# Optimization experiments

Measured on AMD Instinct MI355X. Metric: run time of the kernel, lower is better.

The kernel has to match this reference:

```python
import jax, jax.numpy as jnp
import numpy as np

N_HEADS = 16
ROPE_BASE = 10000.0


def _rope_tables(T, head_dim, dtype):
    inv_freq = 1.0 / (ROPE_BASE ** (jnp.arange(0, head_dim, 2, dtype=jnp.float32) / head_dim))
    t = jnp.arange(T, dtype=jnp.float32)
    freqs = jnp.outer(t, inv_freq)              # (T, head_dim/2)
    emb = jnp.concatenate([freqs, freqs], -1)   # (T, head_dim)
    return jnp.cos(emb).astype(dtype), jnp.sin(emb).astype(dtype)


def _rotate_half(x):
    x1, x2 = jnp.split(x, 2, axis=-1)
    return jnp.concatenate([-x2, x1], axis=-1)


def setup_inputs() -> dict:
    key = jax.random.key(0)
    k1, k2, k3 = jax.random.split(key, 3)
    B, T, C = 2, 2048, 2048
    x = jax.random.normal(k1, (B, T, C), dtype=jnp.float32)
    Wqkv = jax.random.normal(k2, (C, 3 * C), dtype=jnp.float32) * (1.0 / np.sqrt(C))
    Wproj = jax.random.normal(k3, (C, C), dtype=jnp.float32) * (1.0 / np.sqrt(C))
    return {"x": x, "Wqkv": Wqkv, "Wproj": Wproj}


def reference(x, Wqkv, Wproj):
    B, T, C = x.shape
    H = N_HEADS
    D = C // H
    qkv = jnp.einsum('btc,cd->btd', x, Wqkv)            # (B,T,3C)
    q, k, v = jnp.split(qkv, 3, axis=-1)
    # (B,T,C) -> (B,H,T,D)
    q = q.reshape(B, T, H, D).transpose(0, 2, 1, 3)
    k = k.reshape(B, T, H, D).transpose(0, 2, 1, 3)
    v = v.reshape(B, T, H, D).transpose(0, 2, 1, 3)
    cos, sin = _rope_tables(T, D, x.dtype)              # (T,D) each
    q = q * cos + _rotate_half(q) * sin
    k = k * cos + _rotate_half(k) * sin
    scale = 1.0 / jnp.sqrt(jnp.asarray(D, x.dtype))
    att = jnp.einsum('bhqd,bhkd->bhqk', q, k) * scale   # (B,H,T,T)
    causal = jnp.tril(jnp.ones((T, T), dtype=bool))
    att = jnp.where(causal, att, jnp.asarray(-jnp.inf, att.dtype))
    att = jax.nn.softmax(att, axis=-1)
    y = jnp.einsum('bhqk,bhkd->bhqd', att, v)           # (B,H,T,D)
    y = y.transpose(0, 2, 1, 3).reshape(B, T, C)
    return jnp.einsum('btc,cd->btd', y, Wproj)
```

## Files before the change

kernel.cpp:

```cpp
#include <hip/hip_runtime.h>
#include <stdint.h>

#define T_SEQ 2048
#define NH 16
#define HD 128
#define CC 2048
#define N3 6144
#define MM 4096

typedef short bf16x8 __attribute__((ext_vector_type(8)));
typedef float f32x4 __attribute__((ext_vector_type(4)));
typedef float f32x16 __attribute__((ext_vector_type(16)));
typedef unsigned int u32x4 __attribute__((ext_vector_type(4)));

__device__ __forceinline__ unsigned short f2bf(float f) {
  unsigned int u = __float_as_uint(f);
  u += 0x7FFF + ((u >> 16) & 1);
  return (unsigned short)(u >> 16);
}
__device__ __forceinline__ float bf2f(unsigned short h) {
  return __uint_as_float(((unsigned int)h) << 16);
}
__device__ __forceinline__ unsigned int cvt_pk_bf16(float lo, float hi) {
  unsigned int r;
  asm("v_cvt_pk_bf16_f32 %0, %1, %2" : "=v"(r) : "v"(lo), "v"(hi));
  return r;
}

__global__ __launch_bounds__(256) void k_transpose_cvt(const float* __restrict__ in,
                                                       unsigned short* __restrict__ out,
                                                       int K, int N) {
  __shared__ float tile[32][33];
  int k0 = blockIdx.x * 32;
  int n0 = blockIdx.y * 32;
  int tx = threadIdx.x & 31, ty = threadIdx.x >> 5;
  #pragma unroll
  for (int r = ty; r < 32; r += 8)
    tile[r][tx] = in[(size_t)(k0 + r) * N + n0 + tx];
  __syncthreads();
  #pragma unroll
  for (int r = ty; r < 32; r += 8)
    out[(size_t)(n0 + r) * K + k0 + tx] = f2bf(tile[tx][r]);
}

__global__ __launch_bounds__(256) void k_cvt(const float* __restrict__ in,
                                             unsigned short* __restrict__ out, int n4) {
  int i = blockIdx.x * 256 + threadIdx.x;
  if (i >= n4) return;
  float4 v = ((const float4*)in)[i];
  ushort4 o;
  o.x = f2bf(v.x); o.y = f2bf(v.y); o.z = f2bf(v.z); o.w = f2bf(v.w);
  ((ushort4*)out)[i] = o;
}

template<int NJ, int EPI, int MMAJ>
__global__ __launch_bounds__(512, 1) void k_gemm8(const unsigned short* __restrict__ A,
                                                  const unsigned short* __restrict__ Bt,
                                                  float* __restrict__ C,
                                                  unsigned short* __restrict__ qo,
                                                  unsigned short* __restrict__ ko,
                                                  unsigned short* __restrict__ vo,
                                                  int M, int N, int K) {
  constexpr int BU = NJ / 2;
  constexpr int DSTRIDE = (1 + BU) * 16384;
  extern __shared__ __align__(16) char lds[];
  const int tid = threadIdx.x;
  const int lane = tid & 63;
  const int lr = lane & 15, lg = lane >> 4;
  const int wave = tid >> 6;
  const int wm = wave >> 2, wn = wave & 3;
  const int nwg = gridDim.x;
  const int bid = blockIdx.x;
  const int wg = (bid & 7) * (nwg >> 3) + (bid >> 3);
  const int GX = M >> 7;
  const int GN = N / (NJ * 64);
  const int mt = MMAJ ? (wg % GX) : (wg / GN);
  const int nt = MMAJ ? (wg / GX) : (wg % GN);
  const int m0 = mt * 128, n0 = nt * NJ * 64;
  const int NT = K >> 6;

  auto STAGE = [&](int d, int op, int h, int t) {
    const unsigned short* src = op ? Bt : A;
    const int r0 = (op ? n0 + h * 128 : m0);
    const int kc = t * 64;
    char* base = lds + d * DSTRIDE + op * 16384 + h * 16384;
    #pragma unroll
    for (int l = 0; l < 2; ++l) {
      int p = (l * 512 + tid) * 16;
      int qq = p ^ (((p >> 7) & 7) << 4);
      const unsigned short* g = src + (size_t)(r0 + (qq >> 7)) * K + kc + ((qq & 127) >> 1);
      __builtin_amdgcn_global_load_lds(
          (const __attribute__((address_space(1))) void*)g,
          (__attribute__((address_space(3))) void*)(base + (l * 512 + (tid & 448)) * 16),
          16, 0, 0);
    }
  };
  auto RD = [&](int d, int op, int row, int kb) -> bf16x8 {
    const char* base = lds + d * DSTRIDE + op * 16384;
    int p = row * 128 + kb;
    p ^= ((p >> 7) & 7) << 4;
    return *(const bf16x8*)(base + p);
  };

  f32x4 acc[4][NJ];
  #pragma unroll
  for (int i = 0; i < 4; ++i)
    #pragma unroll
    for (int j = 0; j < NJ; ++j) acc[i][j] = (f32x4){0.f, 0.f, 0.f, 0.f};

  bf16x8 bfrg[NJ][2];

#define PHASE(D, MIB, READB, VM, ...)                                                    \
  {                                                                                      \
    if (READB) {                                                                         \
      _Pragma("unroll")                                                                  \
      for (int nj = 0; nj < NJ; ++nj)                                                    \
        _Pragma("unroll")                                                                \
        for (int ks = 0; ks < 2; ++ks)                                                   \
          bfrg[nj][ks] = RD(D, 1, wn * NJ * 16 + nj * 16 + lr, ks * 64 + lg * 16);       \
    }                                                                                    \
    bf16x8 af2[2][2];                                                                    \
    _Pragma("unroll")                                                                    \
    for (int mm = 0; mm < 2; ++mm)                                                       \
      _Pragma("unroll")                                                                  \
      for (int ks = 0; ks < 2; ++ks)                                                     \
        af2[mm][ks] = RD(D, 0, wm * 64 + (MIB + mm) * 16 + lr, ks * 64 + lg * 16);       \
    __VA_ARGS__                                                                          \
    __builtin_amdgcn_s_barrier();                                                        \
    asm volatile("s_waitcnt lgkmcnt(0)" ::: "memory");                                   \
    __builtin_amdgcn_s_setprio(1);                                                       \
    _Pragma("unroll")                                                                    \
    for (int mm = 0; mm < 2; ++mm)                                                       \
      _Pragma("unroll")                                                                  \
      for (int nj = 0; nj < NJ; ++nj)                                                    \
        _Pragma("unroll")                                                                \
        for (int ks = 0; ks < 2; ++ks)                                                   \
          acc[MIB + mm][nj] = __builtin_amdgcn_mfma_f32_16x16x32_bf16(af2[mm][ks], bfrg[nj][ks], acc[MIB + mm][nj], 0, 0, 0); \
    __builtin_amdgcn_s_setprio(0);                                                       \
    if ((VM) == 6) asm volatile("s_waitcnt vmcnt(6)" ::: "memory");                      \
    if ((VM) == 4) asm volatile("s_waitcnt vmcnt(4)" ::: "memory");                      \
    if ((VM) == 2) asm volatile("s_waitcnt vmcnt(2)" ::: "memory");                      \
    __builtin_amdgcn_s_barrier();                                                        \
  }

  const int t1 = NT > 1 ? 1 : 0;
  #pragma unroll
  for (int h = 0; h < BU; ++h) STAGE(0, 1, h, 0);
  STAGE(0, 0, 0, 0);
  #pragma unroll
  for (int h = 0; h < BU; ++h) STAGE(1, 1, h, t1);
  if (NJ == 6) asm volatile("s_waitcnt vmcnt(6)" ::: "memory");
  else         asm volatile("s_waitcnt vmcnt(4)" ::: "memory");
  __builtin_amdgcn_s_barrier();

  for (int it = 0; it < (NT >> 1); ++it) {
    const int tb  = 2 * it + 1;
    const int ta1 = min(2 * it + 2, NT - 1);
    const int tb1 = min(2 * it + 3, NT - 1);
    if (NJ == 6) {
      PHASE(0, 0, true,  -1, STAGE(1, 0, 0, tb);)
      PHASE(0, 2, false,  4, STAGE(0, 1, 0, ta1); STAGE(0, 1, 1, ta1);)
      PHASE(1, 0, true,  -1, STAGE(0, 1, 2, ta1); STAGE(0, 0, 0, ta1);)
      PHASE(1, 2, false,  6, STAGE(1, 1, 0, tb1); STAGE(1, 1, 1, tb1); STAGE(1, 1, 2, tb1);)
    } else {
      PHASE(0, 0, true,  -1, STAGE(1, 0, 0, tb);)
      PHASE(0, 2, false,  2, STAGE(0, 1, 0, ta1);)
      PHASE(1, 0, true,  -1, STAGE(0, 1, 1, ta1); STAGE(0, 0, 0, ta1);)
      PHASE(1, 2, false,  4, STAGE(1, 1, 0, tb1); STAGE(1, 1, 1, tb1);)
    }
  }
#undef PHASE

  #pragma unroll
  for (int mi = 0; mi < 4; ++mi) {
    #pragma unroll
    for (int nj = 0; nj < NJ; ++nj) {
      #pragma unroll
      for (int j = 0; j < 4; ++j) {
        int m = m0 + wm * 64 + mi * 16 + lg * 4 + j;
        int n = n0 + wn * NJ * 16 + nj * 16 + lr;
        float val = acc[mi][nj][j];
        if (EPI == 0) {
          C[(size_t)m * N + n] = val;
        } else {
          int which = n >> 11, cc = n & 2047;
          int h = cc >> 7, d = cc & 127;
          int b = m >> 11, t = m & 2047;
          unsigned short* dst = which == 0 ? qo : (which == 1 ? ko : vo);
          dst[(((size_t)(b * NH + h)) * T_SEQ + t) * HD + d] = f2bf(val);
        }
      }
    }
  }
}

__global__ __launch_bounds__(256) void k_rope(unsigned short* __restrict__ q,
                                              unsigned short* __restrict__ k) {
  int i = blockIdx.x * 256 + threadIdx.x;
  int d = i & 63;
  int t = (i >> 6) & (T_SEQ - 1);
  int bh = i >> 17;
  float invf = exp2f((float)(-2 * d) * (13.287712379549449f / 128.f));
  float ang = (float)t * invf;
  float c = cosf(ang), s = sinf(ang);
  size_t base = ((size_t)bh * T_SEQ + t) * HD + d;
  const float scale = 0.12751741562076117f;
  float q1 = bf2f(q[base]), q2 = bf2f(q[base + 64]);
  q[base]      = f2bf((q1 * c - q2 * s) * scale);
  q[base + 64] = f2bf((q2 * c + q1 * s) * scale);
  float k1 = bf2f(k[base]), k2 = bf2f(k[base + 64]);
  k[base]      = f2bf(k1 * c - k2 * s);
  k[base + 64] = f2bf(k2 * c + k1 * s);
}

__global__ __launch_bounds__(256) void k_transpose_v(const unsigned short* __restrict__ in,
                                                     unsigned short* __restrict__ out) {
  __shared__ unsigned short tile[32][33];
  int bh = blockIdx.z;
  int t0 = blockIdx.x * 32, d0 = blockIdx.y * 32;
  int tx = threadIdx.x & 31, ty = threadIdx.x >> 5;
  const unsigned short* src = in + (size_t)bh * T_SEQ * HD;
  unsigned short* dst = out + (size_t)bh * HD * T_SEQ;
  #pragma unroll
  for (int r = ty; r < 32; r += 8)
    tile[r][tx] = src[(size_t)(t0 + r) * HD + d0 + tx];
  __syncthreads();
  #pragma unroll
  for (int r = ty; r < 32; r += 8)
    dst[(size_t)(d0 + r) * T_SEQ + t0 + tx] = tile[tx][r];
}

__global__ __launch_bounds__(256, 2) void k_attn(const unsigned short* __restrict__ Q,
                                                 const unsigned short* __restrict__ K,
                                                 const unsigned short* __restrict__ Vt,
                                                 unsigned short* __restrict__ Y) {
  __shared__ __align__(16) unsigned short Kls[2][64 * 128];
  __shared__ __align__(16) unsigned short Vls[2][128 * 64];
  const int id = blockIdx.x;
  const int sub = id & 255;
  const int bh = sub & 31;
  const int qtl = (id < 256) ? (15 - (sub >> 5)) : (sub >> 5);
  const int b = bh >> 4, h = bh & 15;
  const int tid = threadIdx.x, wv = tid >> 6, lane = tid & 63;
  const int l31 = lane & 31, hh = lane >> 5;
  const int q0 = qtl * 128;
  const int jtmax = 2 * qtl + 1;
  const int qglob = q0 + wv * 32 + l31;
  const unsigned short* Qb = Q + (size_t)bh * T_SEQ * HD;
  const unsigned short* Kb = K + (size_t)bh * T_SEQ * HD;
  const unsigned short* Vb = Vt + (size_t)bh * HD * T_SEQ;

  auto STAGEKV = [&](int tk, int bb) {
    #pragma unroll
    for (int ch = 0; ch < 4; ++ch) {
      int p = (ch * 256 + tid) * 16;
      int q = p ^ (((p >> 8) & 7) << 4);
      const unsigned short* g = Kb + (size_t)(tk + (q >> 8)) * HD + ((q & 255) >> 1);
      __builtin_amdgcn_global_load_lds(
          (const __attribute__((address_space(1))) void*)g,
          (__attribute__((address_space(3))) void*)((char*)Kls[bb] + (ch * 256 + (tid & 192)) * 16),
          16, 0, 0);
    }
    #pragma unroll
    for (int ch = 0; ch < 4; ++ch) {
      int p = (ch * 256 + tid) * 16;
      int q = p ^ (((p >> 7) & 7) << 4);
      const unsigned short* g = Vb + (size_t)(q >> 7) * T_SEQ + tk + ((q & 127) >> 1);
      __builtin_amdgcn_global_load_lds(
          (const __attribute__((address_space(1))) void*)g,
          (__attribute__((address_space(3))) void*)((char*)Vls[bb] + (ch * 256 + (tid & 192)) * 16),
          16, 0, 0);
    }
  };

  bf16x8 qfr[8];
  #pragma unroll
  for (int c = 0; c < 8; ++c)
    qfr[c] = *(const bf16x8*)(Qb + (size_t)qglob * HD + c * 16 + hh * 8);

  f32x16 oacc[4];
  #pragma unroll
  for (int dt = 0; dt < 4; ++dt)
    #pragma unroll
    for (int r = 0; r < 16; ++r) oacc[dt][r] = 0.f;
  float mrun = -1e30f, lrun = 0.f;

  STAGEKV(0, 0);
  asm volatile("s_waitcnt vmcnt(0)" ::: "memory");
  __syncthreads();

  for (int jt = 0; jt <= jtmax; ++jt) {
    const int cur = jt & 1;
    if (jt < jtmax) STAGEKV((jt + 1) * 64, cur ^ 1);

    f32x16 sacc[2];
    #pragma unroll
    for (int t = 0; t < 2; ++t)
      #pragma unroll
      for (int r = 0; r < 16; ++r) sacc[t][r] = 0.f;
    __builtin_amdgcn_s_setprio(1);
    #pragma unroll
    for (int s = 0; s < 8; ++s) {
      #pragma unroll
      for (int t = 0; t < 2; ++t) {
        int row = t * 32 + l31;
        int byte = (row * 256 + s * 32 + hh * 16) ^ ((row & 7) << 4);
        bf16x8 kf = *(const bf16x8*)((const char*)Kls[cur] + byte);
        sacc[t] = __builtin_amdgcn_mfma_f32_32x32x16_bf16(kf, qfr[s], sacc[t], 0, 0, 0);
      }
    }
    __builtin_amdgcn_s_setprio(0);

    if (jt >= 2 * qtl) {
      #pragma unroll
      for (int t = 0; t < 2; ++t)
        #pragma unroll
        for (int r = 0; r < 16; ++r) {
          int kg = jt * 64 + t * 32 + (r & 3) + 8 * (r >> 2) + 4 * hh;
          if (kg > qglob) sacc[t][r] = -1e30f;
        }
    }

    float pmax = sacc[0][0];
    #pragma unroll
    for (int r = 1; r < 16; ++r) pmax = fmaxf(pmax, sacc[0][r]);
    #pragma unroll
    for (int r = 0; r < 16; ++r) pmax = fmaxf(pmax, sacc[1][r]);
    pmax = fmaxf(pmax, __shfl_xor(pmax, 32));

    if (__any(pmax > mrun + 8.0f)) {
      float mnew = fmaxf(mrun, pmax);
      float osc = exp2f(mrun - mnew);
      lrun *= osc;
      mrun = mnew;
      #pragma unroll
      for (int r = 0; r < 16; ++r) {
        int qr = (r & 3) + 8 * (r >> 2) + 4 * hh;
        float sr = __shfl(osc, qr);
        #pragma unroll
        for (int dt = 0; dt < 4; ++dt) oacc[dt][r] *= sr;
      }
    }

    unsigned int pk[16];
    float rsum = 0.f;
    #pragma unroll
    for (int t = 0; t < 2; ++t)
      #pragma unroll
      for (int i = 0; i < 8; ++i) {
        float p0 = exp2f(sacc[t][2 * i] - mrun);
        float p1 = exp2f(sacc[t][2 * i + 1] - mrun);
        rsum += p0 + p1;
        pk[t * 8 + i] = cvt_pk_bf16(p0, p1);
      }
    rsum += __shfl_xor(rsum, 32);
    lrun += rsum;

    bf16x8 pa[4];
    #pragma unroll
    for (int c = 0; c < 4; ++c) {
      int base = (c >> 1) * 8 + (c & 1) * 4;
      unsigned int s0 = hh == 0 ? pk[base + 2] : pk[base + 0];
      unsigned int s1 = hh == 0 ? pk[base + 3] : pk[base + 1];
      unsigned int r0 = __shfl_xor((int)s0, 32);
      unsigned int r1 = __shfl_xor((int)s1, 32);
      u32x4 f;
      f[0] = hh == 0 ? pk[base + 0] : r0;
      f[1] = hh == 0 ? pk[base + 1] : r1;
      f[2] = hh == 0 ? r0 : pk[base + 2];
      f[3] = hh == 0 ? r1 : pk[base + 3];
      pa[c] = *(bf16x8*)&f;
    }

    __builtin_amdgcn_s_setprio(1);
    #pragma unroll
    for (int dt = 0; dt < 4; ++dt) {
      #pragma unroll
      for (int c = 0; c < 4; ++c) {
        int row = dt * 32 + l31;
        int byte = (row * 128 + c * 32 + hh * 16) ^ ((row & 7) << 4);
        bf16x8 vf = *(const bf16x8*)((const char*)Vls[cur] + byte);
        oacc[dt] = __builtin_amdgcn_mfma_f32_32x32x16_bf16(pa[c], vf, oacc[dt], 0, 0, 0);
      }
    }
    __builtin_amdgcn_s_setprio(0);

    asm volatile("s_waitcnt vmcnt(0)" ::: "memory");
    __syncthreads();
  }

  float linv = 1.0f / lrun;
  #pragma unroll
  for (int r = 0; r < 16; ++r) {
    int qr = (r & 3) + 8 * (r >> 2) + 4 * hh;
    float li = __shfl(linv, qr);
    int qg = q0 + wv * 32 + qr;
    size_t base = ((size_t)b * T_SEQ + qg) * CC + h * HD;
    #pragma unroll
    for (int dt = 0; dt < 4; ++dt)
      Y[base + dt * 32 + l31] = f2bf(oacc[dt][r] * li);
  }
}

extern "C" void kernel_launch(void* const* d_in, const int* in_sizes, int n_in,
                              void* d_out, int out_size, void* d_ws, size_t ws_size,
                              hipStream_t stream) {
  const float* x     = (const float*)d_in[0];
  const float* Wqkv  = (const float*)d_in[1];
  const float* Wproj = (const float*)d_in[2];
  float* out = (float*)d_out;
  char* ws = (char*)d_ws;
  const size_t MB = 1024 * 1024;
  unsigned short* WqkvT  = (unsigned short*)(ws + 0);
  unsigned short* vt     = (unsigned short*)(ws + 0);
  unsigned short* WprojT = (unsigned short*)(ws + 24 * MB);
  unsigned short* xb     = (unsigned short*)(ws + 32 * MB);
  unsigned short* y      = xb;
  unsigned short* q      = (unsigned short*)(ws + 48 * MB);
  unsigned short* k      = (unsigned short*)(ws + 64 * MB);
  unsigned short* v      = (unsigned short*)(ws + 80 * MB);

  k_transpose_cvt<<<dim3(CC / 32, N3 / 32), 256, 0, stream>>>(Wqkv, WqkvT, CC, N3);
  k_transpose_cvt<<<dim3(CC / 32, CC / 32), 256, 0, stream>>>(Wproj, WprojT, CC, CC);
  k_cvt<<<(MM * CC / 4) / 256, 256, 0, stream>>>(x, xb, MM * CC / 4);
  k_gemm8<6, 1, 1><<<dim3((MM / 128) * (N3 / 384)), 512, 131072, stream>>>(
      xb, WqkvT, nullptr, q, k, v, MM, N3, CC);
  k_rope<<<(32 * T_SEQ * 64) / 256, 256, 0, stream>>>(q, k);
  k_transpose_v<<<dim3(T_SEQ / 32, HD / 32, 32), 256, 0, stream>>>(v, vt);
  k_attn<<<dim3(512), 256, 0, stream>>>(q, k, vt, y);
  k_gemm8<4, 0, 0><<<dim3((MM / 128) * (CC / 256)), 512, 98304, stream>>>(
      y, WprojT, out, nullptr, nullptr, nullptr, MM, CC, CC);
}
```

Measured before the change: 266.7 us.

## Software-pipeline PV MMA behind next QK tile and split GEMM phases finer

In the attention kernel, the P·V matrix multiply for the previous key tile is deferred and issued after the current tile's QK scores, so it can overlap with the softmax work. V is triple-buffered in dynamic LDS (80 KB) to support this. The QKV GEMM (NJ=6 variant) splits each phase into single-row-block sub-phases, each interleaving one staging load, to spread global loads more evenly. The larger LDS footprint may reduce attention occupancy below two blocks per CU, and the extra sub-phases add more barriers.

```diff
diff --git a/kernel.cpp b/kernel.cpp
--- a/kernel.cpp
+++ b/kernel.cpp
@@ -110,7 +110,35 @@
 
   bf16x8 bfrg[NJ][2];
 
-#define PHASE(D, MIB, READB, VM, ...)                                                    \
+#define GPH(D, MI, READB, DOST, SD, SO, SH, ST, VM)                                      \
+  {                                                                                      \
+    if (READB) {                                                                         \
+      _Pragma("unroll")                                                                  \
+      for (int nj = 0; nj < NJ; ++nj)                                                    \
+        _Pragma("unroll")                                                                \
+        for (int ks = 0; ks < 2; ++ks)                                                   \
+          bfrg[nj][ks] = RD(D, 1, wn * NJ * 16 + nj * 16 + lr, ks * 64 + lg * 16);       \
+    }                                                                                    \
+    bf16x8 af[2];                                                                        \
+    _Pragma("unroll")                                                                    \
+    for (int ks = 0; ks < 2; ++ks)                                                       \
+      af[ks] = RD(D, 0, wm * 64 + (MI) * 16 + lr, ks * 64 + lg * 16);                    \
+    if (DOST) STAGE(SD, SO, SH, ST);                                                     \
+    __builtin_amdgcn_s_barrier();                                                        \
+    asm volatile("s_waitcnt lgkmcnt(0)" ::: "memory");                                   \
+    __builtin_amdgcn_s_setprio(1);                                                       \
+    _Pragma("unroll")                                                                    \
+    for (int nj = 0; nj < NJ; ++nj)                                                      \
+      _Pragma("unroll")                                                                  \
+      for (int ks = 0; ks < 2; ++ks)                                                     \
+        acc[MI][nj] = __builtin_amdgcn_mfma_f32_16x16x32_bf16(af[ks], bfrg[nj][ks], acc[MI][nj], 0, 0, 0); \
+    __builtin_amdgcn_s_setprio(0);                                                       \
+    if ((VM) == 6) asm volatile("s_waitcnt vmcnt(6)" ::: "memory");                      \
+    if ((VM) == 4) asm volatile("s_waitcnt vmcnt(4)" ::: "memory");                      \
+    __builtin_amdgcn_s_barrier();                                                        \
+  }
+
+#define GPM(D, MIB, READB, VM, ...)                                                      \
   {                                                                                      \
     if (READB) {                                                                         \
       _Pragma("unroll")                                                                  \
@@ -137,7 +165,6 @@
         for (int ks = 0; ks < 2; ++ks)                                                   \
           acc[MIB + mm][nj] = __builtin_amdgcn_mfma_f32_16x16x32_bf16(af2[mm][ks], bfrg[nj][ks], acc[MIB + mm][nj], 0, 0, 0); \
     __builtin_amdgcn_s_setprio(0);                                                       \
-    if ((VM) == 6) asm volatile("s_waitcnt vmcnt(6)" ::: "memory");                      \
     if ((VM) == 4) asm volatile("s_waitcnt vmcnt(4)" ::: "memory");                      \
     if ((VM) == 2) asm volatile("s_waitcnt vmcnt(2)" ::: "memory");                      \
     __builtin_amdgcn_s_barrier();                                                        \
@@ -157,19 +184,24 @@
     const int tb  = 2 * it + 1;
     const int ta1 = min(2 * it + 2, NT - 1);
     const int tb1 = min(2 * it + 3, NT - 1);
-    if (NJ == 6) {
-      PHASE(0, 0, true,  -1, STAGE(1, 0, 0, tb);)
-      PHASE(0, 2, false,  4, STAGE(0, 1, 0, ta1); STAGE(0, 1, 1, ta1);)
-      PHASE(1, 0, true,  -1, STAGE(0, 1, 2, ta1); STAGE(0, 0, 0, ta1);)
-      PHASE(1, 2, false,  6, STAGE(1, 1, 0, tb1); STAGE(1, 1, 1, tb1); STAGE(1, 1, 2, tb1);)
+    if constexpr (NJ == 6) {
+      GPH(0, 0, true,  true, 1, 0, 0, tb,  -1)
+      GPH(0, 1, false, true, 0, 1, 0, ta1, -1)
+      GPH(0, 2, false, true, 0, 1, 1, ta1, -1)
+      GPH(0, 3, false, true, 0, 1, 2, ta1,  6)
+      GPH(1, 0, true,  true, 0, 0, 0, ta1, -1)
+      GPH(1, 1, false, true, 1, 1, 0, tb1, -1)
+      GPH(1, 2, false, true, 1, 1, 1, tb1, -1)
+      GPH(1, 3, false, true, 1, 1, 2, tb1,  6)
     } else {
-      PHASE(0, 0, true,  -1, STAGE(1, 0, 0, tb);)
-      PHASE(0, 2, false,  2, STAGE(0, 1, 0, ta1);)
-      PHASE(1, 0, true,  -1, STAGE(0, 1, 1, ta1); STAGE(0, 0, 0, ta1);)
-      PHASE(1, 2, false,  4, STAGE(1, 1, 0, tb1); STAGE(1, 1, 1, tb1);)
-    }
-  }
-#undef PHASE
+      GPM(0, 0, true,  -1, STAGE(1, 0, 0, tb);)
+      GPM(0, 2, false,  2, STAGE(0, 1, 0, ta1);)
+      GPM(1, 0, true,  -1, STAGE(0, 1, 1, ta1); STAGE(0, 0, 0, ta1);)
+      GPM(1, 2, false,  4, STAGE(1, 1, 0, tb1); STAGE(1, 1, 1, tb1);)
+    }
+  }
+#undef GPH
+#undef GPM
 
   #pragma unroll
   for (int mi = 0; mi < 4; ++mi) {
@@ -234,8 +266,9 @@
                                                  const unsigned short* __restrict__ K,
                                                  const unsigned short* __restrict__ Vt,
                                                  unsigned short* __restrict__ Y) {
-  __shared__ __align__(16) unsigned short Kls[2][64 * 128];
-  __shared__ __align__(16) unsigned short Vls[2][128 * 64];
+  extern __shared__ __align__(16) char alds[];
+  char* Kls = alds;
+  char* Vls = alds + 32768;
   const int id = blockIdx.x;
   const int sub = id & 255;
   const int bh = sub & 31;
@@ -250,7 +283,8 @@
   const unsigned short* Kb = K + (size_t)bh * T_SEQ * HD;
   const unsigned short* Vb = Vt + (size_t)bh * HD * T_SEQ;
 
-  auto STAGEKV = [&](int tk, int bb) {
+  auto STAGEK = [&](int tk, int s) {
+    char* base = Kls + s * 16384;
     #pragma unroll
     for (int ch = 0; ch < 4; ++ch) {
       int p = (ch * 256 + tid) * 16;
@@ -258,9 +292,12 @@
       const unsigned short* g = Kb + (size_t)(tk + (q >> 8)) * HD + ((q & 255) >> 1);
       __builtin_amdgcn_global_load_lds(
           (const __attribute__((address_space(1))) void*)g,
-          (__attribute__((address_space(3))) void*)((char*)Kls[bb] + (ch * 256 + (tid & 192)) * 16),
+          (__attribute__((address_space(3))) void*)(base + (ch * 256 + (tid & 192)) * 16),
           16, 0, 0);
     }
+  };
+  auto STAGEV = [&](int tk, int s) {
+    char* base = Vls + s * 16384;
     #pragma unroll
     for (int ch = 0; ch < 4; ++ch) {
       int p = (ch * 256 + tid) * 16;
@@ -268,7 +305,7 @@
       const unsigned short* g = Vb + (size_t)(q >> 7) * T_SEQ + tk + ((q & 127) >> 1);
       __builtin_amdgcn_global_load_lds(
           (const __attribute__((address_space(1))) void*)g,
-          (__attribute__((address_space(3))) void*)((char*)Vls[bb] + (ch * 256 + (tid & 192)) * 16),
+          (__attribute__((address_space(3))) void*)(base + (ch * 256 + (tid & 192)) * 16),
           16, 0, 0);
     }
   };
@@ -284,32 +321,71 @@
     #pragma unroll
     for (int r = 0; r < 16; ++r) oacc[dt][r] = 0.f;
   float mrun = -1e30f, lrun = 0.f;
-
-  STAGEKV(0, 0);
+  bf16x8 paP0, paP1, paP2, paP3;
+
+#define PV_BLOCK(VBASE_)                                                                 \
+  {                                                                                      \
+    const char* vb_ = (VBASE_);                                                          \
+    __builtin_amdgcn_s_setprio(1);                                                       \
+    _Pragma("unroll")                                                                    \
+    for (int dt = 0; dt < 4; ++dt) {                                                     \
+      _Pragma("unroll")                                                                  \
+      for (int c = 0; c < 4; ++c) {                                                      \
+        bf16x8 pz = (c == 0) ? paP0 : ((c == 1) ? paP1 : ((c == 2) ? paP2 : paP3));      \
+        int row_ = dt * 32 + l31;                                                        \
+        int byte_ = (row_ * 128 + c * 32 + hh * 16) ^ ((row_ & 7) << 4);                 \
+        bf16x8 vf = *(const bf16x8*)(vb_ + byte_);                                       \
+        oacc[dt] = __builtin_amdgcn_mfma_f32_32x32x16_bf16(pz, vf, oacc[dt], 0, 0, 0);   \
+      }                                                                                  \
+    }                                                                                    \
+    __builtin_amdgcn_s_setprio(0);                                                       \
+  }
+
+#define MAKE_PA(c, dst)                                                                  \
+  {                                                                                      \
+    int base_ = ((c) >> 1) * 8 + ((c) & 1) * 4;                                          \
+    unsigned int s0 = hh == 0 ? pk[base_ + 2] : pk[base_ + 0];                           \
+    unsigned int s1 = hh == 0 ? pk[base_ + 3] : pk[base_ + 1];                           \
+    unsigned int r0 = __shfl_xor((int)s0, 32);                                           \
+    unsigned int r1 = __shfl_xor((int)s1, 32);                                           \
+    u32x4 f;                                                                             \
+    f[0] = hh == 0 ? pk[base_ + 0] : r0;                                                 \
+    f[1] = hh == 0 ? pk[base_ + 1] : r1;                                                 \
+    f[2] = hh == 0 ? r0 : pk[base_ + 2];                                                 \
+    f[3] = hh == 0 ? r1 : pk[base_ + 3];                                                 \
+    dst = *(bf16x8*)&f;                                                                  \
+  }
+
+  STAGEK(0, 0); STAGEV(0, 0);
   asm volatile("s_waitcnt vmcnt(0)" ::: "memory");
   __syncthreads();
 
   for (int jt = 0; jt <= jtmax; ++jt) {
-    const int cur = jt & 1;
-    if (jt < jtmax) STAGEKV((jt + 1) * 64, cur ^ 1);
+    const int kcur = jt & 1;
+    const int vnext = (jt + 1) % 3;
+    const int vprev = (jt + 2) % 3;
+    if (jt < jtmax) { STAGEK((jt + 1) * 64, kcur ^ 1); STAGEV((jt + 1) * 64, vnext); }
 
     f32x16 sacc[2];
     #pragma unroll
     for (int t = 0; t < 2; ++t)
       #pragma unroll
       for (int r = 0; r < 16; ++r) sacc[t][r] = 0.f;
-    __builtin_amdgcn_s_setprio(1);
-    #pragma unroll
-    for (int s = 0; s < 8; ++s) {
-      #pragma unroll
-      for (int t = 0; t < 2; ++t) {
-        int row = t * 32 + l31;
-        int byte = (row * 256 + s * 32 + hh * 16) ^ ((row & 7) << 4);
-        bf16x8 kf = *(const bf16x8*)((const char*)Kls[cur] + byte);
-        sacc[t] = __builtin_amdgcn_mfma_f32_32x32x16_bf16(kf, qfr[s], sacc[t], 0, 0, 0);
+    {
+      const char* kbase = Kls + kcur * 16384;
+      __builtin_amdgcn_s_setprio(1);
+      #pragma unroll
+      for (int s = 0; s < 8; ++s) {
+        #pragma unroll
+        for (int t = 0; t < 2; ++t) {
+          int row = t * 32 + l31;
+          int byte = (row * 256 + s * 32 + hh * 16) ^ ((row & 7) << 4);
+          bf16x8 kf = *(const bf16x8*)(kbase + byte);
+          sacc[t] = __builtin_amdgcn_mfma_f32_32x32x16_bf16(kf, qfr[s], sacc[t], 0, 0, 0);
+        }
       }
-    }
-    __builtin_amdgcn_s_setprio(0);
+      __builtin_amdgcn_s_setprio(0);
+    }
 
     if (jt >= 2 * qtl) {
       #pragma unroll
@@ -320,6 +396,8 @@
           if (kg > qglob) sacc[t][r] = -1e30f;
         }
     }
+
+    if (jt > 0) PV_BLOCK(Vls + vprev * 16384)
 
     float pmax = sacc[0][0];
     #pragma unroll
@@ -356,38 +434,16 @@
     rsum += __shfl_xor(rsum, 32);
     lrun += rsum;
 
-    bf16x8 pa[4];
-    #pragma unroll
-    for (int c = 0; c < 4; ++c) {
-      int base = (c >> 1) * 8 + (c & 1) * 4;
-      unsigned int s0 = hh == 0 ? pk[base + 2] : pk[base + 0];
-      unsigned int s1 = hh == 0 ? pk[base + 3] : pk[base + 1];
-      unsigned int r0 = __shfl_xor((int)s0, 32);
-      unsigned int r1 = __shfl_xor((int)s1, 32);
-      u32x4 f;
-      f[0] = hh == 0 ? pk[base + 0] : r0;
-      f[1] = hh == 0 ? pk[base + 1] : r1;
-      f[2] = hh == 0 ? r0 : pk[base + 2];
-      f[3] = hh == 0 ? r1 : pk[base + 3];
-      pa[c] = *(bf16x8*)&f;
-    }
-
-    __builtin_amdgcn_s_setprio(1);
-    #pragma unroll
-    for (int dt = 0; dt < 4; ++dt) {
-      #pragma unroll
-      for (int c = 0; c < 4; ++c) {
-        int row = dt * 32 + l31;
-        int byte = (row * 128 + c * 32 + hh * 16) ^ ((row & 7) << 4);
-        bf16x8 vf = *(const bf16x8*)((const char*)Vls[cur] + byte);
-        oacc[dt] = __builtin_amdgcn_mfma_f32_32x32x16_bf16(pa[c], vf, oacc[dt], 0, 0, 0);
-      }
-    }
-    __builtin_amdgcn_s_setprio(0);
+    MAKE_PA(0, paP0)
+    MAKE_PA(1, paP1)
+    MAKE_PA(2, paP2)
+    MAKE_PA(3, paP3)
 
     asm volatile("s_waitcnt vmcnt(0)" ::: "memory");
     __syncthreads();
   }
+
+  PV_BLOCK(Vls + (jtmax % 3) * 16384)
 
   float linv = 1.0f / lrun;
   #pragma unroll
@@ -400,6 +456,8 @@
     for (int dt = 0; dt < 4; ++dt)
       Y[base + dt * 32 + l31] = f2bf(oacc[dt][r] * li);
   }
+#undef PV_BLOCK
+#undef MAKE_PA
 }
 
 extern "C" void kernel_launch(void* const* d_in, const int* in_sizes, int n_in,
@@ -427,7 +485,7 @@
       xb, WqkvT, nullptr, q, k, v, MM, N3, CC);
   k_rope<<<(32 * T_SEQ * 64) / 256, 256, 0, stream>>>(q, k);
   k_transpose_v<<<dim3(T_SEQ / 32, HD / 32, 32), 256, 0, stream>>>(v, vt);
-  k_attn<<<dim3(512), 256, 0, stream>>>(q, k, vt, y);
+  k_attn<<<dim3(512), 256, 81920, stream>>>(q, k, vt, y);
   k_gemm8<4, 0, 0><<<dim3((MM / 128) * (CC / 256)), 512, 98304, stream>>>(
       y, WprojT, out, nullptr, nullptr, nullptr, MM, CC, CC);
 }
```

Measured after the change: 267.0 us. No clear change (+0.1%).
